# Performance work log

Hardware: AMD Instinct MI355X
Metric: run time of the kernel (lower is better)

Reference implementation:

```python
import jax, jax.numpy as jnp
import numpy as np
from jax import lax

N, H, W, CIN = 64, 256, 256, 3   # batch, image HxW, RGB
C, K = 32, 5                     # cross-conv channels / kernel size (from reshape(-1,32,5,5))
ADIM, AHID = 4, 256              # action dim, action-encoder hidden


def _conv(x, w, b, stride, pad):
    # x [N,C,H,W], w [O,I,kh,kw] (torch OIHW cross-correlation semantics)
    y = lax.conv_general_dilated(x, w, (stride, stride), [(pad, pad), (pad, pad)],
                                 dimension_numbers=('NCHW', 'OIHW', 'NCHW'))
    return y + b[None, :, None, None]


def cross_convolve(feat, kernels):
    # feat [N,C,h,w], kernels [N,C,K,K]; per-sample per-channel 'same' conv (padding=2).
    # Equivalent to the original N*C loop of tiny F.conv2d calls: one depthwise
    # (grouped, feature_group_count=C) conv per sample, vmapped over the batch.
    def one(x, k):  # x [C,h,w], k [C,K,K]
        y = lax.conv_general_dilated(x[None], k[:, None], (1, 1), [(2, 2), (2, 2)],
                                     dimension_numbers=('NCHW', 'OIHW', 'NCHW'),
                                     feature_group_count=C)
        return y[0]
    return jax.vmap(one)(feat, kernels)


def setup_inputs() -> dict:
    key = jax.random.key(0)
    ks = jax.random.split(key, 10)
    g = lambda i, shape, s: jax.random.normal(ks[i], shape, jnp.float32) * s
    return {
        'images': jax.random.normal(ks[0], (N, H, W, CIN), jnp.float32),
        'actions': jax.random.normal(ks[1], (N, ADIM), jnp.float32),
        # phys_encoder: conv(3->32,k5,s2,p2) relu, conv(32->32,k5,s2,p2) relu
        'pe_w1': g(2, (C, CIN, 5, 5), 0.08), 'pe_b1': jnp.zeros((C,), jnp.float32),
        'pe_w2': g(3, (C, C, 5, 5), 0.04), 'pe_b2': jnp.zeros((C,), jnp.float32),
        # action_encoder MLP: ADIM -> AHID -> C*K*K (=800)
        'ae_w1': g(4, (ADIM, AHID), 0.3), 'ae_b1': jnp.zeros((AHID,), jnp.float32),
        'ae_w2': g(5, (AHID, C * K * K), 0.05), 'ae_b2': jnp.zeros((C * K * K,), jnp.float32),
        # motion_predictor: conv(32->32,k3,p1) relu, conv(32->2,k3,p1)
        'mp_w1': g(6, (C, C, 3, 3), 0.06), 'mp_b1': jnp.zeros((C,), jnp.float32),
        'mp_w2': g(7, (2, C, 3, 3), 0.06), 'mp_b2': jnp.zeros((2,), jnp.float32),
    }


def reference(images, actions, pe_w1, pe_b1, pe_w2, pe_b2,
              ae_w1, ae_b1, ae_w2, ae_b2, mp_w1, mp_b1, mp_w2, mp_b2):
    x = jnp.transpose(images, (0, 3, 1, 2))                 # NHWC -> NCHW
    h = jax.nn.relu(_conv(x, pe_w1, pe_b1, 2, 2))           # [N,32,128,128]
    h = jax.nn.relu(_conv(h, pe_w2, pe_b2, 2, 2))           # [N,32,64,64]
    a = jax.nn.relu(actions @ ae_w1 + ae_b1)
    a = (a @ ae_w2 + ae_b2).reshape(-1, C, K, K)            # per-sample kernels [N,32,5,5]
    sa = cross_convolve(h, a)                               # [N,32,64,64]
    f = jax.nn.relu(_conv(sa, mp_w1, mp_b1, 1, 1))
    flow = _conv(f, mp_w2, mp_b2, 1, 1)                     # [N,2,64,64]
    return flow
```

## Files before the change

### kernel.cpp

```cpp
#include <hip/hip_runtime.h>


typedef __attribute__((ext_vector_type(8))) short bf16x8;
typedef __attribute__((ext_vector_type(4))) float f32x4;
typedef __attribute__((ext_vector_type(16))) float f32x16;

__device__ __forceinline__ unsigned short f2bf(float f) {
    unsigned int u = __float_as_uint(f);
    u = (u + 0x7FFFu + ((u >> 16) & 1u)) >> 16;
    return (unsigned short)u;
}
__device__ __forceinline__ float bf2f(unsigned short h) {
    return __uint_as_float(((unsigned int)h) << 16);
}

__global__ __launch_bounds__(64) void zero_border2(unsigned int* t0, int R0, int p0,
                                                   unsigned int* t1, int R1, int p1) {
    unsigned int* t = blockIdx.y ? t1 : t0;
    const int R = blockIdx.y ? R1 : R0;
    const int pad = blockIdx.y ? p1 : p0;
    const int row = blockIdx.x % R;
    const int n = blockIdx.x / R;
    if (n >= 64) return;
    const int tid = threadIdx.x;
    unsigned int* rp = t + (size_t)(n * R + row) * R * 16;
    if (row < pad || row >= R - pad) {
        for (int i = tid; i < R * 16; i += 64) rp[i] = 0u;
    } else {
        for (int i = tid; i < pad * 16; i += 64) {
            rp[i] = 0u;
            rp[(size_t)(R - pad) * 16 + i] = 0u;
        }
    }
}

__global__ __launch_bounds__(256) void pad_img_kernel(const float* __restrict__ img,
                                                      unsigned short* __restrict__ imgp) {
    const int py = blockIdx.x % 260;
    const int n  = blockIdx.x / 260;
    const int iy = py - 2;
    const bool rowok = (iy >= 0) && (iy < 256);
    const float* srow = img + ((size_t)n * 256 + (rowok ? iy : 0)) * 768;
    unsigned short* drow = imgp + (size_t)(n * 260 + py) * 1056;
    for (int s = threadIdx.x; s < 1056; s += 256) {
        int px = s >> 2, c = s & 3;
        int ix = px - 2;
        float v = 0.f;
        if (rowok && c < 3 && ix >= 0 && ix < 256) v = srow[ix * 3 + c];
        drow[s] = f2bf(v);
    }
}

__global__ __launch_bounds__(256) void repack_all(const float* __restrict__ pe_w1,
                                                  const float* __restrict__ pe_w2,
                                                  const float* __restrict__ mp_w1,
                                                  const float* __restrict__ mp_w2,
                                                  unsigned short* __restrict__ B1,
                                                  unsigned short* __restrict__ B2,
                                                  unsigned short* __restrict__ Bm1,
                                                  unsigned short* __restrict__ Bm2) {
    int idx = blockIdx.x * 256 + threadIdx.x;
    if (idx < 5120) {
        int kh = idx / 1024, r = idx % 1024, o = r / 32, k = r % 32, dx = k >> 2, c = k & 3;
        float v = (dx < 5 && c < 3) ? pe_w1[o * 75 + c * 25 + kh * 5 + dx] : 0.f;
        B1[idx] = f2bf(v);
    } else if (idx < 30720) {
        int i = idx - 5120;
        int co = i / 800, r = i % 800, ci = r / 25, tap = r % 25;
        B2[(tap * 32 + co) * 32 + ci] = f2bf(pe_w2[i]);
    } else if (idx < 39936) {
        int i = idx - 30720;
        int co = i / 288, r = i % 288, ci = r / 9, tap = r % 9;
        Bm1[(tap * 32 + co) * 32 + ci] = f2bf(mp_w1[i]);
    } else if (idx < 44544) {
        int i = idx - 39936;
        int tap = i / 512, r = i % 512, co = r / 32, ci = r % 32;
        float v = (co < 2) ? mp_w2[co * 288 + ci * 9 + tap] : 0.f;
        Bm2[i] = f2bf(v);
    }
}

__global__ __launch_bounds__(256) void mlp_kernel(const float* __restrict__ actions,
                                                  const float* __restrict__ w1,
                                                  const float* __restrict__ b1,
                                                  const float* __restrict__ w2,
                                                  const float* __restrict__ b2,
                                                  float* __restrict__ aout) {
    int n = blockIdx.y;
    int t = threadIdx.x;
    __shared__ float hid[256];
    float a0 = actions[n * 4 + 0], a1 = actions[n * 4 + 1];
    float a2 = actions[n * 4 + 2], a3 = actions[n * 4 + 3];
    float acc = b1[t];
    acc += a0 * w1[0 * 256 + t] + a1 * w1[1 * 256 + t] +
           a2 * w1[2 * 256 + t] + a3 * w1[3 * 256 + t];
    hid[t] = fmaxf(acc, 0.0f);
    __syncthreads();
    int o = blockIdx.x * 200 + t;
    if (t < 200) {
        float s = b2[o];
        #pragma unroll 4
        for (int i = 0; i < 256; ++i) s += hid[i] * w2[i * 800 + o];
        aout[n * 800 + o] = s;
    }
}

__global__ __launch_bounds__(256, 4) void conv1_mfma(const unsigned short* __restrict__ imgp,
                                                     const short* __restrict__ B1,
                                                     const float* __restrict__ bias,
                                                     unsigned short* __restrict__ h1p) {
    const int tid = threadIdx.x;
    const int lane = tid & 63;
    const int w = tid >> 6;
    const int n = blockIdx.y;
    const int cohalf = w & 1;
    const int oy = blockIdx.x * 2 + (w >> 1);
    const int ml = lane & 15;
    const int kg = lane >> 4;

    bf16x8 bfrag[5];
    #pragma unroll
    for (int kh = 0; kh < 5; ++kh)
        bfrag[kh] = *(const bf16x8*)(B1 + ((kh * 32 + cohalf * 16 + ml) * 32 + kg * 8));
    const float bia = bias[cohalf * 16 + ml];
    const int co = cohalf * 16 + ml;

    f32x4 acc[8];
    #pragma unroll
    for (int t = 0; t < 8; ++t) acc[t] = (f32x4){bia, bia, bia, bia};

    for (int kh = 0; kh < 5; ++kh) {
        const unsigned short* rowbase = imgp + (size_t)(n * 260 + 2 * oy + kh) * 1056;
        bf16x8 af[8];
        #pragma unroll
        for (int t = 0; t < 8; ++t) {
            const int px0 = 2 * (16 * t + ml) + 2 * kg;
            af[t] = *(const bf16x8*)(rowbase + px0 * 4);
        }
        #pragma unroll
        for (int t = 0; t < 8; ++t)
            acc[t] = __builtin_amdgcn_mfma_f32_16x16x32_bf16(af[t], bfrag[kh], acc[t], 0, 0, 0);
    }
    #pragma unroll
    for (int t = 0; t < 8; ++t) {
        #pragma unroll
        for (int r = 0; r < 4; ++r) {
            const int px = 16 * t + kg * 4 + r;
            h1p[((size_t)(n * 132 + oy + 2) * 132 + px + 2) * 32 + co] = f2bf(fmaxf(acc[t][r], 0.f));
        }
    }
}

__global__ __launch_bounds__(256, 4) void conv2_mfma32(const unsigned short* __restrict__ h1p,
                                                       const unsigned int* __restrict__ B,
                                                       const float* __restrict__ bias,
                                                       unsigned short* __restrict__ h2p) {
    __shared__ unsigned int Bs[5 * 32 * 20];
    const int tid = threadIdx.x;
    const int lane = tid & 63;
    const int w = tid >> 6;
    const int n = blockIdx.y;
    const int oy = blockIdx.x * 2 + (w >> 1);
    const int x0 = (w & 1) * 32;
    const int co = lane & 31;
    const int kgrp = lane >> 5;

    const float bia = bias[co];
    f32x16 acc;
    #pragma unroll
    for (int r = 0; r < 16; ++r) acc[r] = bia;

    const unsigned short* bbase = (const unsigned short*)Bs + co * 40 + kgrp * 8;
    const int px0 = 2 * (x0 + co);

    for (int kh = 0; kh < 5; ++kh) {
        if (kh) __syncthreads();
        const unsigned int* src = B + kh * 2560;
        #pragma unroll
        for (int i = tid; i < 2560; i += 256) {
            int row = i >> 4, p = i & 15;
            Bs[row * 20 + p] = src[i];
        }
        __syncthreads();

        const unsigned short* rowbase = h1p + (size_t)(n * 132 + 2 * oy + kh) * (132 * 32) + kgrp * 8;
        bf16x8 a[10], b[10];
        #pragma unroll
        for (int kw = 0; kw < 5; ++kw) {
            a[2 * kw]     = *(const bf16x8*)(rowbase + (px0 + kw) * 32);
            a[2 * kw + 1] = *(const bf16x8*)(rowbase + (px0 + kw) * 32 + 16);
            b[2 * kw]     = *(const bf16x8*)(bbase + kw * (32 * 40));
            b[2 * kw + 1] = *(const bf16x8*)(bbase + kw * (32 * 40) + 16);
        }
        #pragma unroll
        for (int kw = 0; kw < 5; ++kw) {
            acc = __builtin_amdgcn_mfma_f32_32x32x16_bf16(a[2 * kw], b[2 * kw], acc, 0, 0, 0);
            acc = __builtin_amdgcn_mfma_f32_32x32x16_bf16(a[2 * kw + 1], b[2 * kw + 1], acc, 0, 0, 0);
        }
    }
    #pragma unroll
    for (int r = 0; r < 16; ++r) {
        const int px = (r & 3) + 8 * (r >> 2) + 4 * kgrp;
        const int ox = x0 + px;
        h2p[((size_t)(n * 68 + oy + 2) * 68 + ox + 2) * 32 + co] = f2bf(fmaxf(acc[r], 0.f));
    }
}

__global__ __launch_bounds__(256) void xconv_kernel(const unsigned short* __restrict__ h2p,
                                                    const float* __restrict__ ker,
                                                    unsigned short* __restrict__ sap) {
    __shared__ __align__(16) unsigned short tile[12 * 68 * 32];
    const int tid = threadIdx.x;
    const int n = blockIdx.x;
    const int rb = blockIdx.y;
    const unsigned short* src = h2p + (size_t)(n * 68 + rb * 8) * (68 * 32);
    for (int i = tid; i < 3264; i += 256)
        *(uint4*)(tile + i * 8) = *(const uint4*)(src + i * 8);
    const int ci = tid & 31, xg = tid >> 5;
    const float* kp = ker + (size_t)(n * 32 + ci) * 25;
    float k[25];
    #pragma unroll
    for (int t = 0; t < 25; ++t) k[t] = kp[t];
    __syncthreads();

    float acc[8][8];
    #pragma unroll
    for (int r = 0; r < 8; ++r)
        #pragma unroll
        for (int j = 0; j < 8; ++j) acc[r][j] = 0.f;

    #pragma unroll
    for (int ir = 0; ir < 12; ++ir) {
        float v[12];
        #pragma unroll
        for (int t = 0; t < 12; ++t)
            v[t] = bf2f(tile[(ir * 68 + xg * 8 + t) * 32 + ci]);
        #pragma unroll
        for (int kh = 0; kh < 5; ++kh) {
            const int r = ir - kh;
            if (r >= 0 && r < 8) {
                #pragma unroll
                for (int j = 0; j < 8; ++j) {
                    float s = acc[r][j];
                    #pragma unroll
                    for (int kw = 0; kw < 5; ++kw) s += k[kh * 5 + kw] * v[j + kw];
                    acc[r][j] = s;
                }
            }
        }
    }
    #pragma unroll
    for (int r = 0; r < 8; ++r)
        #pragma unroll
        for (int j = 0; j < 8; ++j)
            sap[((size_t)(n * 66 + rb * 8 + r + 1) * 66 + xg * 8 + j + 1) * 32 + ci] = f2bf(acc[r][j]);
}

__global__ __launch_bounds__(256, 5) void mp1_mfma32(const unsigned short* __restrict__ sap,
                                                     const unsigned int* __restrict__ B,
                                                     const float* __restrict__ bias,
                                                     unsigned short* __restrict__ fp) {
    __shared__ unsigned int Bs[9 * 32 * 20];
    const int tid = threadIdx.x;
    #pragma unroll
    for (int i = tid; i < 4608; i += 256) {
        int row = i >> 4, p = i & 15;
        Bs[row * 20 + p] = B[i];
    }
    __syncthreads();

    const int lane = tid & 63;
    const int w = tid >> 6;
    const int n = blockIdx.y;
    const int oy = blockIdx.x * 2 + (w >> 1);
    const int x0 = (w & 1) * 32;
    const int co = lane & 31;
    const int kgrp = lane >> 5;

    const float bia = bias[co];
    f32x16 acc;
    #pragma unroll
    for (int r = 0; r < 16; ++r) acc[r] = bia;

    const unsigned short* bbase = (const unsigned short*)Bs + co * 40 + kgrp * 8;
    const int px0 = x0 + co;

    for (int kh = 0; kh < 3; ++kh) {
        const unsigned short* rowbase = sap + (size_t)(n * 66 + oy + kh) * (66 * 32) + kgrp * 8;
        bf16x8 a[6], b[6];
        #pragma unroll
        for (int kw = 0; kw < 3; ++kw) {
            const int tap = kh * 3 + kw;
            a[2 * kw]     = *(const bf16x8*)(rowbase + (px0 + kw) * 32);
            a[2 * kw + 1] = *(const bf16x8*)(rowbase + (px0 + kw) * 32 + 16);
            b[2 * kw]     = *(const bf16x8*)(bbase + tap * (32 * 40));
            b[2 * kw + 1] = *(const bf16x8*)(bbase + tap * (32 * 40) + 16);
        }
        #pragma unroll
        for (int kw = 0; kw < 3; ++kw) {
            acc = __builtin_amdgcn_mfma_f32_32x32x16_bf16(a[2 * kw], b[2 * kw], acc, 0, 0, 0);
            acc = __builtin_amdgcn_mfma_f32_32x32x16_bf16(a[2 * kw + 1], b[2 * kw + 1], acc, 0, 0, 0);
        }
    }
    #pragma unroll
    for (int r = 0; r < 16; ++r) {
        const int px = (r & 3) + 8 * (r >> 2) + 4 * kgrp;
        const int ox = x0 + px;
        fp[((size_t)(n * 66 + oy + 1) * 66 + ox + 1) * 32 + co] = f2bf(fmaxf(acc[r], 0.f));
    }
}

__global__ __launch_bounds__(256, 4) void mp2_mfma(const unsigned short* __restrict__ fpb,
                                                   const short* __restrict__ B,
                                                   const float* __restrict__ bias,
                                                   float* __restrict__ out) {
    const int tid = threadIdx.x;
    const int lane = tid & 63;
    const int w = tid >> 6;
    const int n = blockIdx.y;
    const int oy = blockIdx.x * 4 + w;
    const int ml = lane & 15;
    const int kg = lane >> 4;

    bf16x8 bfrag[9];
    #pragma unroll
    for (int t = 0; t < 9; ++t)
        bfrag[t] = *(const bf16x8*)(B + ((t * 16 + ml) * 32 + kg * 8));
    const float bia = (ml < 2) ? bias[ml] : 0.f;

    f32x4 acc[4];
    #pragma unroll
    for (int t = 0; t < 4; ++t) acc[t] = (f32x4){bia, bia, bia, bia};

    for (int kh = 0; kh < 3; ++kh) {
        const unsigned short* rowbase = fpb + (size_t)(n * 66 + oy + kh) * (66 * 32);
        bf16x8 af[12];
        #pragma unroll
        for (int kw = 0; kw < 3; ++kw)
            #pragma unroll
            for (int t = 0; t < 4; ++t)
                af[kw * 4 + t] = *(const bf16x8*)(rowbase + (16 * t + ml + kw) * 32 + kg * 8);
        #pragma unroll
        for (int kw = 0; kw < 3; ++kw)
            #pragma unroll
            for (int t = 0; t < 4; ++t)
                acc[t] = __builtin_amdgcn_mfma_f32_16x16x32_bf16(af[kw * 4 + t], bfrag[kh * 3 + kw], acc[t], 0, 0, 0);
    }
    if (ml < 2) {
        #pragma unroll
        for (int t = 0; t < 4; ++t) {
            #pragma unroll
            for (int r = 0; r < 4; ++r) {
                const int px = 16 * t + kg * 4 + r;
                out[(size_t)n * 8192 + (size_t)ml * 4096 + (size_t)oy * 64 + px] = acc[t][r];
            }
        }
    }
}

extern "C" void kernel_launch(void* const* d_in, const int* in_sizes, int n_in,
                              void* d_out, int out_size, void* d_ws, size_t ws_size,
                              hipStream_t stream) {
    (void)in_sizes; (void)n_in; (void)out_size; (void)ws_size;
    const float* images  = (const float*)d_in[0];
    const float* actions = (const float*)d_in[1];
    const float* pe_w1   = (const float*)d_in[2];
    const float* pe_b1   = (const float*)d_in[3];
    const float* pe_w2   = (const float*)d_in[4];
    const float* pe_b2   = (const float*)d_in[5];
    const float* ae_w1   = (const float*)d_in[6];
    const float* ae_b1   = (const float*)d_in[7];
    const float* ae_w2   = (const float*)d_in[8];
    const float* ae_b2   = (const float*)d_in[9];
    const float* mp_w1   = (const float*)d_in[10];
    const float* mp_b1   = (const float*)d_in[11];
    const float* mp_w2   = (const float*)d_in[12];
    const float* mp_b2   = (const float*)d_in[13];
    float* out = (float*)d_out;

    char* ws = (char*)d_ws;
    float* a_ker          = (float*)(ws + 0);
    unsigned short* B1    = (unsigned short*)(ws + 204800);
    unsigned short* B2    = (unsigned short*)(ws + 215040);
    unsigned short* Bm1   = (unsigned short*)(ws + 266240);
    unsigned short* Bm2   = (unsigned short*)(ws + 284672);
    unsigned short* h1p   = (unsigned short*)(ws + 524288);
    unsigned short* imgp  = (unsigned short*)(ws + 71892992);
    unsigned short* h2p   = (unsigned short*)(ws + 71892992);
    unsigned short* sap   = (unsigned short*)(ws + 90832896);
    unsigned short* fpb   = (unsigned short*)(ws + 108675072);

    repack_all<<<174, 256, 0, stream>>>(pe_w1, pe_w2, mp_w1, mp_w2, B1, B2, Bm1, Bm2);
    mlp_kernel<<<dim3(4, 64), 256, 0, stream>>>(actions, ae_w1, ae_b1, ae_w2, ae_b2, a_ker);
    zero_border2<<<dim3(64 * 132, 2), 64, 0, stream>>>((unsigned int*)h1p, 132, 2,
                                                       (unsigned int*)fpb, 66, 1);

    pad_img_kernel<<<64 * 260, 256, 0, stream>>>(images, imgp);
    conv1_mfma<<<dim3(64, 64), 256, 0, stream>>>(imgp, (const short*)B1, pe_b1, h1p);

    zero_border2<<<dim3(64 * 68, 2), 64, 0, stream>>>((unsigned int*)h2p, 68, 2,
                                                      (unsigned int*)sap, 66, 1);

    conv2_mfma32<<<dim3(32, 64), 256, 0, stream>>>(h1p, (const unsigned int*)B2, pe_b2, h2p);
    xconv_kernel<<<dim3(64, 8), 256, 0, stream>>>(h2p, a_ker, sap);
    mp1_mfma32<<<dim3(32, 64), 256, 0, stream>>>(sap, (const unsigned int*)Bm1, mp_b1, fpb);
    mp2_mfma<<<dim3(16, 64), 256, 0, stream>>>(fpb, (const short*)Bm2, mp_b2, out);
}
```

Baseline: 288.0 us.

## Split conv1 output into even/odd column planes and dual-accumulate MFMA chains

conv1 now writes its activation into separate even- and odd-column padded buffers. The stride-2 conv2 can then read contiguous pixels instead of gathering every other pixel. conv2 and mp1 split their MFMA accumulation into two independent accumulators, which shortens the dependent MFMA chain, and they load B fragments from shared memory just in time instead of holding them all in registers. Sched barriers and unrolled kh loops are added across the conv kernels, and mp1's occupancy hint drops from 5 to 4, which trades register budget against waves per SIMD.

```diff
diff --git a/kernel.cpp b/kernel.cpp
--- a/kernel.cpp
+++ b/kernel.cpp
@@ -31,6 +31,20 @@
             rp[i] = 0u;
             rp[(size_t)(R - pad) * 16 + i] = 0u;
         }
+    }
+}
+
+__global__ __launch_bounds__(64) void zero_border_eo(unsigned int* E, unsigned int* O) {
+    unsigned int* t = blockIdx.y ? O : E;
+    const int row = blockIdx.x % 132;
+    const int n = blockIdx.x / 132;
+    const int tid = threadIdx.x;
+    unsigned int* rp = t + (size_t)(n * 132 + row) * (66 * 16);
+    if (row < 2 || row >= 130) {
+        for (int i = tid; i < 66 * 16; i += 64) rp[i] = 0u;
+    } else if (tid < 16) {
+        rp[tid] = 0u;
+        rp[65 * 16 + tid] = 0u;
     }
 }
 
@@ -108,7 +122,8 @@
 __global__ __launch_bounds__(256, 4) void conv1_mfma(const unsigned short* __restrict__ imgp,
                                                      const short* __restrict__ B1,
                                                      const float* __restrict__ bias,
-                                                     unsigned short* __restrict__ h1p) {
+                                                     unsigned short* __restrict__ h1e,
+                                                     unsigned short* __restrict__ h1o) {
     const int tid = threadIdx.x;
     const int lane = tid & 63;
     const int w = tid >> 6;
@@ -129,6 +144,7 @@
     #pragma unroll
     for (int t = 0; t < 8; ++t) acc[t] = (f32x4){bia, bia, bia, bia};
 
+    #pragma unroll
     for (int kh = 0; kh < 5; ++kh) {
         const unsigned short* rowbase = imgp + (size_t)(n * 260 + 2 * oy + kh) * 1056;
         bf16x8 af[8];
@@ -137,21 +153,26 @@
             const int px0 = 2 * (16 * t + ml) + 2 * kg;
             af[t] = *(const bf16x8*)(rowbase + px0 * 4);
         }
+        __builtin_amdgcn_sched_barrier(0);
         #pragma unroll
         for (int t = 0; t < 8; ++t)
             acc[t] = __builtin_amdgcn_mfma_f32_16x16x32_bf16(af[t], bfrag[kh], acc[t], 0, 0, 0);
     }
+    const size_t rowoff = ((size_t)(n * 132) + oy + 2) * 2112 + co;
     #pragma unroll
     for (int t = 0; t < 8; ++t) {
         #pragma unroll
         for (int r = 0; r < 4; ++r) {
             const int px = 16 * t + kg * 4 + r;
-            h1p[((size_t)(n * 132 + oy + 2) * 132 + px + 2) * 32 + co] = f2bf(fmaxf(acc[t][r], 0.f));
-        }
-    }
-}
-
-__global__ __launch_bounds__(256, 4) void conv2_mfma32(const unsigned short* __restrict__ h1p,
+            const unsigned short v = f2bf(fmaxf(acc[t][r], 0.f));
+            if ((r & 1) == 0) h1e[rowoff + (size_t)((px + 2) >> 1) * 32] = v;
+            else              h1o[rowoff + (size_t)((px + 1) >> 1) * 32] = v;
+        }
+    }
+}
+
+__global__ __launch_bounds__(256, 4) void conv2_mfma32(const unsigned short* __restrict__ h1e,
+                                                       const unsigned short* __restrict__ h1o,
                                                        const unsigned int* __restrict__ B,
                                                        const float* __restrict__ bias,
                                                        unsigned short* __restrict__ h2p) {
@@ -162,16 +183,16 @@
     const int n = blockIdx.y;
     const int oy = blockIdx.x * 2 + (w >> 1);
     const int x0 = (w & 1) * 32;
-    const int co = lane & 31;
+    const int ml = lane & 31;
     const int kgrp = lane >> 5;
 
-    const float bia = bias[co];
-    f32x16 acc;
-    #pragma unroll
-    for (int r = 0; r < 16; ++r) acc[r] = bia;
-
-    const unsigned short* bbase = (const unsigned short*)Bs + co * 40 + kgrp * 8;
-    const int px0 = 2 * (x0 + co);
+    const float bia = bias[ml];
+    f32x16 accA, accB;
+    #pragma unroll
+    for (int r = 0; r < 16; ++r) { accA[r] = bia; accB[r] = 0.f; }
+
+    const unsigned short* bbase = (const unsigned short*)Bs + ml * 40 + kgrp * 8;
+    const int qbase = (x0 + ml) * 32 + kgrp * 8;
 
     for (int kh = 0; kh < 5; ++kh) {
         if (kh) __syncthreads();
@@ -183,26 +204,42 @@
         }
         __syncthreads();
 
-        const unsigned short* rowbase = h1p + (size_t)(n * 132 + 2 * oy + kh) * (132 * 32) + kgrp * 8;
-        bf16x8 a[10], b[10];
-        #pragma unroll
-        for (int kw = 0; kw < 5; ++kw) {
-            a[2 * kw]     = *(const bf16x8*)(rowbase + (px0 + kw) * 32);
-            a[2 * kw + 1] = *(const bf16x8*)(rowbase + (px0 + kw) * 32 + 16);
-            b[2 * kw]     = *(const bf16x8*)(bbase + kw * (32 * 40));
-            b[2 * kw + 1] = *(const bf16x8*)(bbase + kw * (32 * 40) + 16);
-        }
-        #pragma unroll
-        for (int kw = 0; kw < 5; ++kw) {
-            acc = __builtin_amdgcn_mfma_f32_32x32x16_bf16(a[2 * kw], b[2 * kw], acc, 0, 0, 0);
-            acc = __builtin_amdgcn_mfma_f32_32x32x16_bf16(a[2 * kw + 1], b[2 * kw + 1], acc, 0, 0, 0);
+        const size_t rowoff = ((size_t)(n * 132) + 2 * oy + kh) * 2112;
+        const unsigned short* re = h1e + rowoff + qbase;
+        const unsigned short* ro = h1o + rowoff + qbase;
+        bf16x8 ae[6], ao[4];
+        #pragma unroll
+        for (int j = 0; j < 3; ++j) {
+            ae[2 * j]     = *(const bf16x8*)(re + j * 32);
+            ae[2 * j + 1] = *(const bf16x8*)(re + j * 32 + 16);
+        }
+        #pragma unroll
+        for (int j = 0; j < 2; ++j) {
+            ao[2 * j]     = *(const bf16x8*)(ro + j * 32);
+            ao[2 * j + 1] = *(const bf16x8*)(ro + j * 32 + 16);
+        }
+        __builtin_amdgcn_sched_barrier(0);
+        #pragma unroll
+        for (int j = 0; j < 3; ++j) {
+            const bf16x8 b0 = *(const bf16x8*)(bbase + (2 * j) * 1280);
+            const bf16x8 b1 = *(const bf16x8*)(bbase + (2 * j) * 1280 + 16);
+            accA = __builtin_amdgcn_mfma_f32_32x32x16_bf16(ae[2 * j], b0, accA, 0, 0, 0);
+            accA = __builtin_amdgcn_mfma_f32_32x32x16_bf16(ae[2 * j + 1], b1, accA, 0, 0, 0);
+        }
+        #pragma unroll
+        for (int j = 0; j < 2; ++j) {
+            const bf16x8 b0 = *(const bf16x8*)(bbase + (2 * j + 1) * 1280);
+            const bf16x8 b1 = *(const bf16x8*)(bbase + (2 * j + 1) * 1280 + 16);
+            accB = __builtin_amdgcn_mfma_f32_32x32x16_bf16(ao[2 * j], b0, accB, 0, 0, 0);
+            accB = __builtin_amdgcn_mfma_f32_32x32x16_bf16(ao[2 * j + 1], b1, accB, 0, 0, 0);
         }
     }
     #pragma unroll
     for (int r = 0; r < 16; ++r) {
         const int px = (r & 3) + 8 * (r >> 2) + 4 * kgrp;
         const int ox = x0 + px;
-        h2p[((size_t)(n * 68 + oy + 2) * 68 + ox + 2) * 32 + co] = f2bf(fmaxf(acc[r], 0.f));
+        h2p[((size_t)(n * 68 + oy + 2) * 68 + ox + 2) * 32 + ml] =
+            f2bf(fmaxf(accA[r] + accB[r], 0.f));
     }
 }
 
@@ -256,7 +293,7 @@
             sap[((size_t)(n * 66 + rb * 8 + r + 1) * 66 + xg * 8 + j + 1) * 32 + ci] = f2bf(acc[r][j]);
 }
 
-__global__ __launch_bounds__(256, 5) void mp1_mfma32(const unsigned short* __restrict__ sap,
+__global__ __launch_bounds__(256, 4) void mp1_mfma32(const unsigned short* __restrict__ sap,
                                                      const unsigned int* __restrict__ B,
                                                      const float* __restrict__ bias,
                                                      unsigned short* __restrict__ fp) {
@@ -274,39 +311,47 @@
     const int n = blockIdx.y;
     const int oy = blockIdx.x * 2 + (w >> 1);
     const int x0 = (w & 1) * 32;
-    const int co = lane & 31;
+    const int ml = lane & 31;
     const int kgrp = lane >> 5;
 
-    const float bia = bias[co];
-    f32x16 acc;
-    #pragma unroll
-    for (int r = 0; r < 16; ++r) acc[r] = bia;
-
-    const unsigned short* bbase = (const unsigned short*)Bs + co * 40 + kgrp * 8;
-    const int px0 = x0 + co;
-
+    const float bia = bias[ml];
+    f32x16 accA, accB;
+    #pragma unroll
+    for (int r = 0; r < 16; ++r) { accA[r] = bia; accB[r] = 0.f; }
+
+    const unsigned short* bbase = (const unsigned short*)Bs + ml * 40 + kgrp * 8;
+    const int px0 = x0 + ml;
+
+    #pragma unroll
     for (int kh = 0; kh < 3; ++kh) {
-        const unsigned short* rowbase = sap + (size_t)(n * 66 + oy + kh) * (66 * 32) + kgrp * 8;
-        bf16x8 a[6], b[6];
+        const unsigned short* rowbase = sap + (size_t)(n * 66 + oy + kh) * 2112 + kgrp * 8;
+        bf16x8 a[6];
+        #pragma unroll
+        for (int kw = 0; kw < 3; ++kw) {
+            a[2 * kw]     = *(const bf16x8*)(rowbase + (px0 + kw) * 32);
+            a[2 * kw + 1] = *(const bf16x8*)(rowbase + (px0 + kw) * 32 + 16);
+        }
+        __builtin_amdgcn_sched_barrier(0);
         #pragma unroll
         for (int kw = 0; kw < 3; ++kw) {
             const int tap = kh * 3 + kw;
-            a[2 * kw]     = *(const bf16x8*)(rowbase + (px0 + kw) * 32);
-            a[2 * kw + 1] = *(const bf16x8*)(rowbase + (px0 + kw) * 32 + 16);
-            b[2 * kw]     = *(const bf16x8*)(bbase + tap * (32 * 40));
-            b[2 * kw + 1] = *(const bf16x8*)(bbase + tap * (32 * 40) + 16);
-        }
-        #pragma unroll
-        for (int kw = 0; kw < 3; ++kw) {
-            acc = __builtin_amdgcn_mfma_f32_32x32x16_bf16(a[2 * kw], b[2 * kw], acc, 0, 0, 0);
-            acc = __builtin_amdgcn_mfma_f32_32x32x16_bf16(a[2 * kw + 1], b[2 * kw + 1], acc, 0, 0, 0);
+            const bf16x8 b0 = *(const bf16x8*)(bbase + tap * 1280);
+            const bf16x8 b1 = *(const bf16x8*)(bbase + tap * 1280 + 16);
+            if (tap & 1) {
+                accB = __builtin_amdgcn_mfma_f32_32x32x16_bf16(a[2 * kw], b0, accB, 0, 0, 0);
+                accB = __builtin_amdgcn_mfma_f32_32x32x16_bf16(a[2 * kw + 1], b1, accB, 0, 0, 0);
+            } else {
+                accA = __builtin_amdgcn_mfma_f32_32x32x16_bf16(a[2 * kw], b0, accA, 0, 0, 0);
+                accA = __builtin_amdgcn_mfma_f32_32x32x16_bf16(a[2 * kw + 1], b1, accA, 0, 0, 0);
+            }
         }
     }
     #pragma unroll
     for (int r = 0; r < 16; ++r) {
         const int px = (r & 3) + 8 * (r >> 2) + 4 * kgrp;
         const int ox = x0 + px;
-        fp[((size_t)(n * 66 + oy + 1) * 66 + ox + 1) * 32 + co] = f2bf(fmaxf(acc[r], 0.f));
+        fp[((size_t)(n * 66 + oy + 1) * 66 + ox + 1) * 32 + ml] =
+            f2bf(fmaxf(accA[r] + accB[r], 0.f));
     }
 }
 
@@ -332,6 +377,7 @@
     #pragma unroll
     for (int t = 0; t < 4; ++t) acc[t] = (f32x4){bia, bia, bia, bia};
 
+    #pragma unroll
     for (int kh = 0; kh < 3; ++kh) {
         const unsigned short* rowbase = fpb + (size_t)(n * 66 + oy + kh) * (66 * 32);
         bf16x8 af[12];
@@ -340,6 +386,7 @@
             #pragma unroll
             for (int t = 0; t < 4; ++t)
                 af[kw * 4 + t] = *(const bf16x8*)(rowbase + (16 * t + ml + kw) * 32 + kg * 8);
+        __builtin_amdgcn_sched_barrier(0);
         #pragma unroll
         for (int kw = 0; kw < 3; ++kw)
             #pragma unroll
@@ -384,7 +431,8 @@
     unsigned short* B2    = (unsigned short*)(ws + 215040);
     unsigned short* Bm1   = (unsigned short*)(ws + 266240);
     unsigned short* Bm2   = (unsigned short*)(ws + 284672);
-    unsigned short* h1p   = (unsigned short*)(ws + 524288);
+    unsigned short* h1e   = (unsigned short*)(ws + 524288);
+    unsigned short* h1o   = (unsigned short*)(ws + 36208640);
     unsigned short* imgp  = (unsigned short*)(ws + 71892992);
     unsigned short* h2p   = (unsigned short*)(ws + 71892992);
     unsigned short* sap   = (unsigned short*)(ws + 90832896);
@@ -392,16 +440,17 @@
 
     repack_all<<<174, 256, 0, stream>>>(pe_w1, pe_w2, mp_w1, mp_w2, B1, B2, Bm1, Bm2);
     mlp_kernel<<<dim3(4, 64), 256, 0, stream>>>(actions, ae_w1, ae_b1, ae_w2, ae_b2, a_ker);
-    zero_border2<<<dim3(64 * 132, 2), 64, 0, stream>>>((unsigned int*)h1p, 132, 2,
-                                                       (unsigned int*)fpb, 66, 1);
+    zero_border_eo<<<dim3(64 * 132, 2), 64, 0, stream>>>((unsigned int*)h1e, (unsigned int*)h1o);
+    zero_border2<<<dim3(64 * 66, 1), 64, 0, stream>>>((unsigned int*)fpb, 66, 1,
+                                                      (unsigned int*)fpb, 66, 1);
 
     pad_img_kernel<<<64 * 260, 256, 0, stream>>>(images, imgp);
-    conv1_mfma<<<dim3(64, 64), 256, 0, stream>>>(imgp, (const short*)B1, pe_b1, h1p);
+    conv1_mfma<<<dim3(64, 64), 256, 0, stream>>>(imgp, (const short*)B1, pe_b1, h1e, h1o);
 
     zero_border2<<<dim3(64 * 68, 2), 64, 0, stream>>>((unsigned int*)h2p, 68, 2,
                                                       (unsigned int*)sap, 66, 1);
 
-    conv2_mfma32<<<dim3(32, 64), 256, 0, stream>>>(h1p, (const unsigned int*)B2, pe_b2, h2p);
+    conv2_mfma32<<<dim3(32, 64), 256, 0, stream>>>(h1e, h1o, (const unsigned int*)B2, pe_b2, h2p);
     xconv_kernel<<<dim3(64, 8), 256, 0, stream>>>(h2p, a_ker, sap);
     mp1_mfma32<<<dim3(32, 64), 256, 0, stream>>>(sap, (const unsigned int*)Bm1, mp_b1, fpb);
     mp2_mfma<<<dim3(16, 64), 256, 0, stream>>>(fpb, (const short*)Bm2, mp_b2, out);
```

Measured after the change: 279.5 us. -2.9%, faster.
